# Kernel tuning notes

Measured on AMD Instinct MI355X. Metric: run time of the kernel, lower is better.

Reference implementation:

```python
import jax, jax.numpy as jnp
import numpy as np

D_MODEL = 512
D_ATTN = 128


def setup_inputs() -> dict:
    key = jax.random.key(0)
    k1, k2, k3, k4, k5 = jax.random.split(key, 5)
    B, N = 4, 4096
    x = jax.random.normal(k1, (B, N, D_MODEL), dtype=jnp.float32)
    key_mask = jnp.ones((B, N, 1), dtype=jnp.float32)
    # nn.Linear params (stored as [in, out] for x @ W)
    W_qkv = jax.random.normal(k2, (D_MODEL, 3 * D_ATTN), dtype=jnp.float32) / np.sqrt(D_MODEL)
    b_qkv = jax.random.normal(k3, (3 * D_ATTN,), dtype=jnp.float32) * 0.01
    W_out = jax.random.normal(k4, (D_ATTN, D_MODEL), dtype=jnp.float32) / np.sqrt(D_ATTN)
    b_out = jax.random.normal(k5, (D_MODEL,), dtype=jnp.float32) * 0.01
    return {"x": x, "key_mask": key_mask, "W_qkv": W_qkv, "b_qkv": b_qkv,
            "W_out": W_out, "b_out": b_out}


def reference(x, key_mask, W_qkv, b_qkv, W_out, b_out):
    # Fused QKV projection: [B, N, 3*d_attn]
    qkv = jnp.einsum('bnd,de->bne', x, W_qkv) + b_qkv
    q, k, v = jnp.split(qkv, 3, axis=-1)  # each [B, N, d_attn]
    d_attn = q.shape[-1]
    scale = 1.0 / np.sqrt(d_attn)
    # Full [B, N, N] score matrix (faithful to original einsum)
    scores = jnp.einsum('bnd,bmd->bnm', q, k)
    # Causal mask applied BEFORE scaling (as in original: mask, then *scale)
    N = x.shape[1]
    causal = jnp.tril(jnp.ones((N, N), dtype=bool))  # True = keep
    scores = jnp.where(causal[None, :, :], scores, -jnp.inf)
    scores = scores * scale
    attn = jax.nn.softmax(scores, axis=-1)  # dropout is identity in eval
    out = jnp.einsum('bnm,bmd->bnd', attn, v)
    out = out * key_mask  # broadcast [B, N, 1]
    out = jnp.einsum('bnd,de->bne', out, W_out) + b_out
    return out
```

## Files before the change

kernel.cpp:

```cpp
#include <hip/hip_runtime.h>
#include <hip/hip_bf16.h>
#include <math.h>

typedef __attribute__((ext_vector_type(4))) float f32x4;
typedef __attribute__((ext_vector_type(4))) float fvec4;
typedef __attribute__((ext_vector_type(8))) short bf16x8_t;
typedef __attribute__((ext_vector_type(4))) short bf16x4_t;

static constexpr int BATCH = 4;
static constexpr int SEQ = 4096;
static constexpr int DM = 512;
static constexpr int DA = 128;
static constexpr int BN = BATCH * SEQ;
static constexpr int IPB = 187;
static constexpr int N_ITEMS = BATCH * IPB;

static constexpr float MASKV = -3.0e38f;
static constexpr float MINIT = -1.0e30f;

static __device__ __forceinline__ unsigned short f2bf(float f) {
  unsigned u = __builtin_bit_cast(unsigned, f);
  u += 0x7fffu + ((u >> 16) & 1u);
  return (unsigned short)(u >> 16);
}
static __device__ __forceinline__ float bf2f(unsigned short u) {
  return __builtin_bit_cast(float, ((unsigned)u) << 16);
}
static __device__ __forceinline__ float fexp2(float x) {
#if __has_builtin(__builtin_amdgcn_exp2f)
  return __builtin_amdgcn_exp2f(x);
#else
  return exp2f(x);
#endif
}
static __device__ __forceinline__ unsigned pkbf(float lo, float hi) {
  unsigned r;
  asm("v_cvt_pk_bf16_f32 %0, %1, %2" : "=v"(r) : "v"(lo), "v"(hi));
  return r;
}

#define GLDS16(gsrc, ldst)                                                        \
  __builtin_amdgcn_global_load_lds(                                               \
      (const __attribute__((address_space(1))) void*)(gsrc),                      \
      (__attribute__((address_space(3))) void*)(ldst), 16, 0, 0)

static constexpr float QSC = 0.08838834764831845f * 1.4426950408889634f;

__global__ __launch_bounds__(256) void prep_kernel(
    const float* __restrict__ x, const float* __restrict__ Wqkv,
    const float* __restrict__ Wout, unsigned short* __restrict__ xbf,
    unsigned short* __restrict__ WqT, unsigned short* __restrict__ WoT) {
  long long i = ((long long)blockIdx.x * 256 + threadIdx.x) * 8;
  if (i < (long long)BN * DM) {
    fvec4 a = *(const fvec4*)&x[i];
    fvec4 b = *(const fvec4*)&x[i + 4];
    union { bf16x8_t v; unsigned short u[8]; } pk;
    pk.u[0] = f2bf(a[0]); pk.u[1] = f2bf(a[1]); pk.u[2] = f2bf(a[2]); pk.u[3] = f2bf(a[3]);
    pk.u[4] = f2bf(b[0]); pk.u[5] = f2bf(b[1]); pk.u[6] = f2bf(b[2]); pk.u[7] = f2bf(b[3]);
    *(bf16x8_t*)&xbf[i] = pk.v;
  }
  int t = blockIdx.x * 256 + threadIdx.x;
  if (t < 512 * 384) {
    int k = t / 384, n = t - k * 384;
    WqT[n * 512 + k] = f2bf(Wqkv[t]);
  }
  if (t < 128 * 512) {
    int k = t >> 9, n = t & 511;
    WoT[n * 128 + k] = f2bf(Wout[t]);
  }
}

__global__ __launch_bounds__(512, 4) void qkv_kernel(
    const unsigned short* __restrict__ xbf, const unsigned short* __restrict__ WqT,
    const float* __restrict__ bias, unsigned short* __restrict__ qbf,
    unsigned short* __restrict__ kpk, unsigned short* __restrict__ vpk) {
  __shared__ unsigned short Alds[128 * 64];
  __shared__ unsigned short Blds[128 * 64];

  const int m0 = blockIdx.x * 128;
  const int n0 = blockIdx.y * 128;
  const int tid = threadIdx.x;
  const int wave = tid >> 6, lane = tid & 63;
  const int g = lane >> 4, lr = lane & 15;
  const int wm = wave >> 2, wn = wave & 3;

  const int srow = lane >> 3;
  const int sslot = lane & 7;
  const int sksw = ((sslot ^ srow) * 8);

  f32x4 acc[4][2] = {};

  for (int kb = 0; kb < DM; kb += 64) {
    __syncthreads();
#pragma unroll
    for (int i = 0; i < 2; ++i) {
      int ch = wave * 2 + i;
      GLDS16(&xbf[(size_t)(m0 + ch * 8 + srow) * DM + kb + sksw],
             (char*)Alds + ch * 1024);
      GLDS16(&WqT[(size_t)(n0 + ch * 8 + srow) * DM + kb + sksw],
             (char*)Blds + ch * 1024);
    }
    asm volatile("s_waitcnt vmcnt(0)" ::: "memory");
    __syncthreads();

#pragma unroll
    for (int c2 = 0; c2 < 2; ++c2) {
      bf16x8_t ar[4], br[2];
#pragma unroll
      for (int mi = 0; mi < 4; ++mi) {
        int row = wm * 64 + mi * 16 + lr;
        ar[mi] = *(const bf16x8_t*)&Alds[row * 64 + (((c2 * 4 + g) ^ (row & 7)) * 8)];
      }
#pragma unroll
      for (int ni = 0; ni < 2; ++ni) {
        int row = wn * 32 + ni * 16 + lr;
        br[ni] = *(const bf16x8_t*)&Blds[row * 64 + (((c2 * 4 + g) ^ (row & 7)) * 8)];
      }
#pragma unroll
      for (int mi = 0; mi < 4; ++mi)
#pragma unroll
        for (int ni = 0; ni < 2; ++ni)
          acc[mi][ni] = __builtin_amdgcn_mfma_f32_16x16x32_bf16(ar[mi], br[ni],
                                                                acc[mi][ni], 0, 0, 0);
    }
  }

  if (n0 == 0) {
#pragma unroll
    for (int ni = 0; ni < 2; ++ni) {
      int col = wn * 32 + ni * 16 + lr;
      float bv = bias[col];
#pragma unroll
      for (int mi = 0; mi < 4; ++mi) {
        int tokb = m0 + wm * 64 + mi * 16 + 4 * g;
#pragma unroll
        for (int r = 0; r < 4; ++r)
          qbf[(size_t)(tokb + r) * DA + col] = f2bf((acc[mi][ni][r] + bv) * QSC);
      }
    }
  } else if (n0 == 128) {
#pragma unroll
    for (int ni = 0; ni < 2; ++ni) {
      int kd = wn * 32 + ni * 16 + lr;
      float bv = bias[128 + kd];
      int unit = (kd >> 5) * 4 + ((kd >> 3) & 3);
      int elem = kd & 7;
#pragma unroll
      for (int mi = 0; mi < 4; ++mi) {
        int tokb = m0 + wm * 64 + mi * 16 + 4 * g;
#pragma unroll
        for (int r = 0; r < 4; ++r) {
          int token = tokb + r;
          int tile32 = token >> 5;
          int u = (((token >> 4) & 1) * 16) + unit;
          kpk[(size_t)tile32 * 4096 + u * 128 + (token & 15) * 8 + elem] =
              f2bf(acc[mi][ni][r] + bv);
        }
      }
    }
  } else {
#pragma unroll
    for (int mi = 0; mi < 4; ++mi) {
      int keyb = m0 + wm * 64 + mi * 16 + 4 * g;
      int tile32 = keyb >> 5;
      int kl0 = keyb & 31;
      int gp = (kl0 >> 2) & 3;
      int jhi = kl0 >> 4;
#pragma unroll
      for (int ni = 0; ni < 2; ++ni) {
        int d = wn * 32 + ni * 16 + lr;
        float bv = bias[256 + d];
        union { bf16x4_t v; unsigned short u[4]; } pk;
#pragma unroll
        for (int r = 0; r < 4; ++r) pk.u[r] = f2bf(acc[mi][ni][r] + bv);
        int unit = (d >> 4) * 4 + gp;
        *(bf16x4_t*)&vpk[(size_t)tile32 * 4096 + unit * 128 + (d & 15) * 8 + jhi * 4] =
            pk.v;
      }
    }
  }
}

static __device__ __forceinline__ void softmax64(
    f32x4 s[4], float& m_r, float& l_r, f32x4* oacc, bf16x8_t pb[2]) {
  float tmax = MASKV;
#pragma unroll
  for (int ct = 0; ct < 4; ++ct)
#pragma unroll
    for (int r = 0; r < 4; ++r) tmax = fmaxf(tmax, s[ct][r]);
  tmax = fmaxf(tmax, __shfl_xor(tmax, 16, 64));
  tmax = fmaxf(tmax, __shfl_xor(tmax, 32, 64));
  if (!__all(tmax <= m_r + 10.0f)) {
    float mn = fmaxf(m_r, tmax);
    float al = fexp2(m_r - mn);
    m_r = mn;
    l_r *= al;
#pragma unroll
    for (int t = 0; t < 8; ++t)
#pragma unroll
      for (int r = 0; r < 4; ++r) oacc[t][r] *= al;
  }
  float rs = 0.f;
#pragma unroll
  for (int ct = 0; ct < 4; ++ct)
#pragma unroll
    for (int r = 0; r < 4; ++r) {
      float p = fexp2(s[ct][r] - m_r);
      s[ct][r] = p;
      rs += p;
    }
  rs += __shfl_xor(rs, 16, 64);
  rs += __shfl_xor(rs, 32, 64);
  l_r += rs;
#pragma unroll
  for (int h = 0; h < 2; ++h) {
    union { unsigned u[4]; bf16x8_t v; } pk;
    pk.u[0] = pkbf(s[2 * h][0], s[2 * h][1]);
    pk.u[1] = pkbf(s[2 * h][2], s[2 * h][3]);
    pk.u[2] = pkbf(s[2 * h + 1][0], s[2 * h + 1][1]);
    pk.u[3] = pkbf(s[2 * h + 1][2], s[2 * h + 1][3]);
    pb[h] = pk.v;
  }
}

__global__ __launch_bounds__(256, 3) void attn_kernel(
    const unsigned short* __restrict__ qbf, const unsigned short* __restrict__ kpk,
    const unsigned short* __restrict__ vpk, const float* __restrict__ key_mask,
    unsigned short* __restrict__ part_o, float* __restrict__ part_ml,
    unsigned short* __restrict__ ctx) {
  __shared__ unsigned short Klds[2][8192];
  __shared__ unsigned short Vlds[8192];

  const int flat = blockIdx.x;
  const int b = flat & 3;
  const int idxr = flat >> 2;
  int rem = idxr;
  int qb = 31;
  for (;;) {
    int nc = (qb + 3) / 3;
    if (rem < nc) break;
    rem -= nc;
    --qb;
  }
  const int ci = rem;
  const bool direct = (qb < 3);
  const int key0 = ci * 384;
  const int nkeys = min(384, (qb + 1) * 128 - key0);
  const int nt = nkeys >> 6;

  const int tid = threadIdx.x;
  const int wave = tid >> 6, lane = tid & 63;
  const int g = lane >> 4, lr = lane & 15;
  const int q0 = wave * 16 + lr;
  const int q1 = q0 + 64;

  bf16x8_t qf0[4], qf1[4];
  {
    const unsigned short* qbase = qbf + ((size_t)(b * SEQ + qb * 128)) * DA + g * 8;
#pragma unroll
    for (int c = 0; c < 4; ++c) {
      qf0[c] = *(const bf16x8_t*)(qbase + (size_t)q0 * DA + c * 32);
      qf1[c] = *(const bf16x8_t*)(qbase + (size_t)q1 * DA + c * 32);
    }
  }

  f32x4 oacc0[8] = {}, oacc1[8] = {};
  float m0r = MINIT, l0 = 0.f, m1r = MINIT, l1 = 0.f;

  const int t32b = b * 128 + ci * 12;
  const unsigned short* ksrc = kpk + (size_t)t32b * 4096 + wave * 2048 + lane * 8;
  const unsigned short* vsrc = vpk + (size_t)t32b * 4096 + wave * 2048 + lane * 8;

#define STAGEK(buf, tt)                                                      \
  do {                                                                       \
    char* kd_ = (char*)Klds[buf] + wave * 4096;                              \
    _Pragma("unroll")                                                        \
    for (int i_ = 0; i_ < 4; ++i_)                                           \
      GLDS16(ksrc + (size_t)(tt) * 8192 + i_ * 512, kd_ + i_ * 1024);        \
  } while (0)
#define STAGEV(tt)                                                           \
  do {                                                                       \
    char* vd_ = (char*)Vlds + wave * 4096;                                   \
    _Pragma("unroll")                                                        \
    for (int i_ = 0; i_ < 4; ++i_)                                           \
      GLDS16(vsrc + (size_t)(tt) * 8192 + i_ * 512, vd_ + i_ * 1024);        \
  } while (0)

  STAGEK(0, 0);

  for (int tt = 0; tt < nt; ++tt) {
    const int cur = tt & 1;
    STAGEV(tt);
    if (tt + 1 < nt) {
      STAGEK(cur ^ 1, tt + 1);
      asm volatile("s_waitcnt vmcnt(8)" ::: "memory");
    } else {
      asm volatile("s_waitcnt vmcnt(4)" ::: "memory");
    }
    __builtin_amdgcn_s_barrier();
    __builtin_amdgcn_sched_barrier(0);

    f32x4 s0[4] = {}, s1[4] = {};
    __builtin_amdgcn_s_setprio(1);
#pragma unroll
    for (int ct = 0; ct < 4; ++ct)
#pragma unroll
      for (int c = 0; c < 4; ++c) {
        bf16x8_t kf = *(const bf16x8_t*)&Klds[cur][(ct >> 1) * 4096 +
                                                   (((ct & 1) * 16 + c * 4 + g) * 16 + lr) * 8];
        s0[ct] = __builtin_amdgcn_mfma_f32_16x16x32_bf16(kf, qf0[c], s0[ct], 0, 0, 0);
        s1[ct] = __builtin_amdgcn_mfma_f32_16x16x32_bf16(kf, qf1[c], s1[ct], 0, 0, 0);
      }
    __builtin_amdgcn_s_setprio(0);

    const int koff = key0 + tt * 64 - qb * 128;
    if (koff + 63 > wave * 16) {
      int thr = q0 - koff;
#pragma unroll
      for (int ct = 0; ct < 4; ++ct)
#pragma unroll
        for (int r = 0; r < 4; ++r)
          if (16 * ct + 4 * g + r > thr) s0[ct][r] = MASKV;
    }
    if (koff + 63 > 64 + wave * 16) {
      int thr = q1 - koff;
#pragma unroll
      for (int ct = 0; ct < 4; ++ct)
#pragma unroll
        for (int r = 0; r < 4; ++r)
          if (16 * ct + 4 * g + r > thr) s1[ct][r] = MASKV;
    }

    bf16x8_t pb0[2], pb1[2];
    softmax64(s0, m0r, l0, oacc0, pb0);
    softmax64(s1, m1r, l1, oacc1, pb1);

    if (tt + 1 < nt) {
      asm volatile("s_waitcnt vmcnt(4)" ::: "memory");
    } else {
      asm volatile("s_waitcnt vmcnt(0)" ::: "memory");
    }
    __builtin_amdgcn_s_barrier();
    __builtin_amdgcn_sched_barrier(0);

    __builtin_amdgcn_s_setprio(1);
#pragma unroll
    for (int t = 0; t < 8; ++t)
#pragma unroll
      for (int h = 0; h < 2; ++h) {
        bf16x8_t vf = *(const bf16x8_t*)&Vlds[h * 4096 + ((t * 4 + g) * 16 + lr) * 8];
        oacc0[t] = __builtin_amdgcn_mfma_f32_16x16x32_bf16(vf, pb0[h], oacc0[t], 0, 0, 0);
        oacc1[t] = __builtin_amdgcn_mfma_f32_16x16x32_bf16(vf, pb1[h], oacc1[t], 0, 0, 0);
      }
    __builtin_amdgcn_s_setprio(0);

    __builtin_amdgcn_s_barrier();
  }
#undef STAGEK
#undef STAGEV

  const int slot = b * IPB + idxr;
#pragma unroll
  for (int grp = 0; grp < 2; ++grp) {
    const int row = grp ? q1 : q0;
    const f32x4* oa = grp ? oacc1 : oacc0;
    const float mr = grp ? m1r : m0r;
    const float lr_ = grp ? l1 : l0;
    if (direct) {
      float km = key_mask[b * SEQ + qb * 128 + row];
      float inv = km / lr_;
      unsigned short* co = ctx + ((size_t)(b * SEQ + qb * 128 + row)) * DA;
#pragma unroll
      for (int t = 0; t < 8; ++t) {
        union { bf16x4_t v; unsigned short u[4]; } pk;
#pragma unroll
        for (int r = 0; r < 4; ++r) pk.u[r] = f2bf(oa[t][r] * inv);
        *(bf16x4_t*)&co[t * 16 + 4 * g] = pk.v;
      }
    } else {
      unsigned short* po = part_o + (size_t)slot * 16384 + (size_t)row * 128;
#pragma unroll
      for (int t = 0; t < 8; ++t) {
        union { bf16x4_t v; unsigned short u[4]; } pk;
#pragma unroll
        for (int r = 0; r < 4; ++r) pk.u[r] = f2bf(oa[t][r]);
        *(bf16x4_t*)&po[t * 16 + 4 * g] = pk.v;
      }
      if (g == 0) {
        float2 ml = make_float2(mr, lr_);
        *(float2*)&part_ml[((size_t)slot * 128 + row) * 2] = ml;
      }
    }
  }
}

__global__ __launch_bounds__(512) void combine_kernel(
    const unsigned short* __restrict__ part_o, const float* __restrict__ part_ml,
    const float* __restrict__ key_mask, unsigned short* __restrict__ ctx) {
  const int qb = 3 + blockIdx.x;
  const int b = blockIdx.y;
  const int nc = (qb + 3) / 3;
  int idx0 = 0;
  for (int q = 31; q > qb; --q) idx0 += (q + 3) / 3;
  const int row = threadIdx.x >> 2, cg = threadIdx.x & 3;

  float m = MINIT;
  for (int ci = 0; ci < nc; ++ci) {
    int slot = b * IPB + idx0 + ci;
    m = fmaxf(m, part_ml[((size_t)slot * 128 + row) * 2 + 0]);
  }
  float l = 0.f;
  float acc[32];
#pragma unroll
  for (int k = 0; k < 32; ++k) acc[k] = 0.f;
  for (int ci = 0; ci < nc; ++ci) {
    int slot = b * IPB + idx0 + ci;
    float mi = part_ml[((size_t)slot * 128 + row) * 2 + 0];
    float li = part_ml[((size_t)slot * 128 + row) * 2 + 1];
    float w = fexp2(mi - m);
    l += w * li;
    const unsigned short* po = part_o + (size_t)slot * 16384 + (size_t)row * 128 + cg * 32;
#pragma unroll
    for (int k8 = 0; k8 < 4; ++k8) {
      bf16x8_t v = *(const bf16x8_t*)(po + k8 * 8);
#pragma unroll
      for (int jj = 0; jj < 8; ++jj)
        acc[k8 * 8 + jj] += w * bf2f((unsigned short)v[jj]);
    }
  }
  int rowg = b * SEQ + qb * 128 + row;
  float sc = key_mask[rowg] / l;
  unsigned short* co = ctx + (size_t)rowg * 128 + cg * 32;
#pragma unroll
  for (int k8 = 0; k8 < 4; ++k8) {
    union { bf16x8_t v; unsigned short u[8]; } pk;
#pragma unroll
    for (int jj = 0; jj < 8; ++jj) pk.u[jj] = f2bf(acc[k8 * 8 + jj] * sc);
    *(bf16x8_t*)(co + k8 * 8) = pk.v;
  }
}

__global__ __launch_bounds__(256) void outproj_kernel(
    const unsigned short* __restrict__ ctx, const unsigned short* __restrict__ WoT,
    const float* __restrict__ bias, float* __restrict__ out) {
  __shared__ unsigned short Alds[64 * 32];
  __shared__ unsigned short Blds[64 * 32];

  const int m0 = blockIdx.x * 64;
  const int n0 = blockIdx.y * 64;
  const int tid = threadIdx.x;
  const int wave = tid >> 6, lane = tid & 63;
  const int g = lane >> 4, lr = lane & 15;
  const int sar = tid >> 2, sak = tid & 3;
  const int sbc = tid & 63, sbk = tid >> 6;

  f32x4 acc[4] = {};

  for (int kb = 0; kb < DA; kb += 32) {
    __syncthreads();
    {
      bf16x8_t v = *(const bf16x8_t*)&ctx[(size_t)(m0 + sar) * DA + kb + sak * 8];
      *(bf16x8_t*)&Alds[(((sar >> 4) * 4 + sak) * 16 + (sar & 15)) * 8] = v;
    }
    {
      bf16x8_t v = *(const bf16x8_t*)&WoT[(size_t)(n0 + sbc) * DA + kb + sbk * 8];
      *(bf16x8_t*)&Blds[(((sbc >> 4) * 4 + sbk) * 16 + (sbc & 15)) * 8] = v;
    }
    __syncthreads();
    bf16x8_t af = *(const bf16x8_t*)&Alds[((wave * 4 + g) * 16 + lr) * 8];
#pragma unroll
    for (int c = 0; c < 4; ++c) {
      bf16x8_t bfr = *(const bf16x8_t*)&Blds[((c * 4 + g) * 16 + lr) * 8];
      acc[c] = __builtin_amdgcn_mfma_f32_16x16x32_bf16(af, bfr, acc[c], 0, 0, 0);
    }
  }

  const int rowb = m0 + wave * 16 + g * 4;
#pragma unroll
  for (int c = 0; c < 4; ++c) {
    int col = n0 + c * 16 + lr;
    float bv = bias[col];
#pragma unroll
    for (int r = 0; r < 4; ++r)
      out[(size_t)(rowb + r) * DM + col] = acc[c][r] + bv;
  }
}

extern "C" void kernel_launch(void* const* d_in, const int* in_sizes, int n_in,
                              void* d_out, int out_size, void* d_ws, size_t ws_size,
                              hipStream_t stream) {
  const float* x = (const float*)d_in[0];
  const float* key_mask = (const float*)d_in[1];
  const float* W_qkv = (const float*)d_in[2];
  const float* b_qkv = (const float*)d_in[3];
  const float* W_out = (const float*)d_in[4];
  const float* b_out = (const float*)d_in[5];
  float* out = (float*)d_out;

  unsigned short* ws = (unsigned short*)d_ws;
  unsigned short* qbf = ws;
  unsigned short* kpk = qbf + (size_t)BN * DA;
  unsigned short* vpk = kpk + (size_t)BN * DA;
  unsigned short* ctx = vpk + (size_t)BN * DA;
  unsigned short* xbf = ctx + (size_t)BN * DA;
  unsigned short* WqT = xbf + (size_t)BN * DM;
  unsigned short* WoT = WqT + (size_t)384 * 512;
  unsigned short* part_o = WoT + (size_t)512 * 128;
  float* part_ml = (float*)(part_o + (size_t)N_ITEMS * 16384);

  prep_kernel<<<dim3((BN * DM / 8 + 255) / 256), 256, 0, stream>>>(
      x, W_qkv, W_out, xbf, WqT, WoT);
  qkv_kernel<<<dim3(BN / 128, 3), 512, 0, stream>>>(xbf, WqT, b_qkv, qbf, kpk, vpk);
  attn_kernel<<<dim3(N_ITEMS), 256, 0, stream>>>(qbf, kpk, vpk, key_mask,
                                                 part_o, part_ml, ctx);
  combine_kernel<<<dim3(29, 4), 512, 0, stream>>>(part_o, part_ml, key_mask, ctx);
  outproj_kernel<<<dim3(BN / 64, 8), 256, 0, stream>>>(ctx, WoT, b_out, out);
}
```

Before: 84.74 us.

## Widen combine parallelism and retile output projection to 128x128 with swizzled async LDS loads

```diff
diff --git a/kernel.cpp b/kernel.cpp
--- a/kernel.cpp
+++ b/kernel.cpp
@@ -397,12 +397,14 @@
 __global__ __launch_bounds__(512) void combine_kernel(
     const unsigned short* __restrict__ part_o, const float* __restrict__ part_ml,
     const float* __restrict__ key_mask, unsigned short* __restrict__ ctx) {
-  const int qb = 3 + blockIdx.x;
+  const int qb = 3 + (blockIdx.x >> 2);
+  const int rq = blockIdx.x & 3;
   const int b = blockIdx.y;
   const int nc = (qb + 3) / 3;
   int idx0 = 0;
   for (int q = 31; q > qb; --q) idx0 += (q + 3) / 3;
-  const int row = threadIdx.x >> 2, cg = threadIdx.x & 3;
+  const int row = rq * 32 + (threadIdx.x >> 4);
+  const int cs = threadIdx.x & 15;
 
   float m = MINIT;
   for (int ci = 0; ci < nc; ++ci) {
@@ -410,79 +412,94 @@
     m = fmaxf(m, part_ml[((size_t)slot * 128 + row) * 2 + 0]);
   }
   float l = 0.f;
-  float acc[32];
-#pragma unroll
-  for (int k = 0; k < 32; ++k) acc[k] = 0.f;
+  float acc[8];
+#pragma unroll
+  for (int k = 0; k < 8; ++k) acc[k] = 0.f;
   for (int ci = 0; ci < nc; ++ci) {
     int slot = b * IPB + idx0 + ci;
     float mi = part_ml[((size_t)slot * 128 + row) * 2 + 0];
     float li = part_ml[((size_t)slot * 128 + row) * 2 + 1];
     float w = fexp2(mi - m);
     l += w * li;
-    const unsigned short* po = part_o + (size_t)slot * 16384 + (size_t)row * 128 + cg * 32;
-#pragma unroll
-    for (int k8 = 0; k8 < 4; ++k8) {
-      bf16x8_t v = *(const bf16x8_t*)(po + k8 * 8);
-#pragma unroll
-      for (int jj = 0; jj < 8; ++jj)
-        acc[k8 * 8 + jj] += w * bf2f((unsigned short)v[jj]);
-    }
+    const unsigned short* po =
+        part_o + (size_t)slot * 16384 + (size_t)row * 128 + cs * 8;
+    bf16x8_t v = *(const bf16x8_t*)po;
+#pragma unroll
+    for (int jj = 0; jj < 8; ++jj) acc[jj] += w * bf2f((unsigned short)v[jj]);
   }
   int rowg = b * SEQ + qb * 128 + row;
   float sc = key_mask[rowg] / l;
-  unsigned short* co = ctx + (size_t)rowg * 128 + cg * 32;
-#pragma unroll
-  for (int k8 = 0; k8 < 4; ++k8) {
-    union { bf16x8_t v; unsigned short u[8]; } pk;
-#pragma unroll
-    for (int jj = 0; jj < 8; ++jj) pk.u[jj] = f2bf(acc[k8 * 8 + jj] * sc);
-    *(bf16x8_t*)(co + k8 * 8) = pk.v;
-  }
-}
-
-__global__ __launch_bounds__(256) void outproj_kernel(
+  union { bf16x8_t v; unsigned short u[8]; } pk;
+#pragma unroll
+  for (int jj = 0; jj < 8; ++jj) pk.u[jj] = f2bf(acc[jj] * sc);
+  *(bf16x8_t*)&ctx[(size_t)rowg * 128 + cs * 8] = pk.v;
+}
+
+__global__ __launch_bounds__(512, 4) void outproj_kernel(
     const unsigned short* __restrict__ ctx, const unsigned short* __restrict__ WoT,
     const float* __restrict__ bias, float* __restrict__ out) {
-  __shared__ unsigned short Alds[64 * 32];
-  __shared__ unsigned short Blds[64 * 32];
-
-  const int m0 = blockIdx.x * 64;
-  const int n0 = blockIdx.y * 64;
+  __shared__ unsigned short Alds[128 * 64];
+  __shared__ unsigned short Blds[128 * 64];
+
+  const int m0 = blockIdx.x * 128;
+  const int n0 = blockIdx.y * 128;
   const int tid = threadIdx.x;
   const int wave = tid >> 6, lane = tid & 63;
   const int g = lane >> 4, lr = lane & 15;
-  const int sar = tid >> 2, sak = tid & 3;
-  const int sbc = tid & 63, sbk = tid >> 6;
-
-  f32x4 acc[4] = {};
-
-  for (int kb = 0; kb < DA; kb += 32) {
+  const int wm = wave >> 2, wn = wave & 3;
+
+  const int srow = lane >> 3;
+  const int sslot = lane & 7;
+  const int sksw = ((sslot ^ srow) * 8);
+
+  f32x4 acc[4][2] = {};
+
+  for (int kb = 0; kb < DA; kb += 64) {
     __syncthreads();
-    {
-      bf16x8_t v = *(const bf16x8_t*)&ctx[(size_t)(m0 + sar) * DA + kb + sak * 8];
-      *(bf16x8_t*)&Alds[(((sar >> 4) * 4 + sak) * 16 + (sar & 15)) * 8] = v;
-    }
-    {
-      bf16x8_t v = *(const bf16x8_t*)&WoT[(size_t)(n0 + sbc) * DA + kb + sbk * 8];
-      *(bf16x8_t*)&Blds[(((sbc >> 4) * 4 + sbk) * 16 + (sbc & 15)) * 8] = v;
-    }
+#pragma unroll
+    for (int i = 0; i < 2; ++i) {
+      int ch = wave * 2 + i;
+      GLDS16(&ctx[(size_t)(m0 + ch * 8 + srow) * DA + kb + sksw],
+             (char*)Alds + ch * 1024);
+      GLDS16(&WoT[(size_t)(n0 + ch * 8 + srow) * DA + kb + sksw],
+             (char*)Blds + ch * 1024);
+    }
+    asm volatile("s_waitcnt vmcnt(0)" ::: "memory");
     __syncthreads();
-    bf16x8_t af = *(const bf16x8_t*)&Alds[((wave * 4 + g) * 16 + lr) * 8];
-#pragma unroll
-    for (int c = 0; c < 4; ++c) {
-      bf16x8_t bfr = *(const bf16x8_t*)&Blds[((c * 4 + g) * 16 + lr) * 8];
-      acc[c] = __builtin_amdgcn_mfma_f32_16x16x32_bf16(af, bfr, acc[c], 0, 0, 0);
-    }
-  }
-
-  const int rowb = m0 + wave * 16 + g * 4;
-#pragma unroll
-  for (int c = 0; c < 4; ++c) {
-    int col = n0 + c * 16 + lr;
+
+#pragma unroll
+    for (int c2 = 0; c2 < 2; ++c2) {
+      bf16x8_t ar[4], br[2];
+#pragma unroll
+      for (int mi = 0; mi < 4; ++mi) {
+        int row = wm * 64 + mi * 16 + lr;
+        ar[mi] = *(const bf16x8_t*)&Alds[row * 64 + (((c2 * 4 + g) ^ (row & 7)) * 8)];
+      }
+#pragma unroll
+      for (int ni = 0; ni < 2; ++ni) {
+        int row = wn * 32 + ni * 16 + lr;
+        br[ni] = *(const bf16x8_t*)&Blds[row * 64 + (((c2 * 4 + g) ^ (row & 7)) * 8)];
+      }
+#pragma unroll
+      for (int mi = 0; mi < 4; ++mi)
+#pragma unroll
+        for (int ni = 0; ni < 2; ++ni)
+          acc[mi][ni] = __builtin_amdgcn_mfma_f32_16x16x32_bf16(ar[mi], br[ni],
+                                                                acc[mi][ni], 0, 0, 0);
+    }
+  }
+
+#pragma unroll
+  for (int ni = 0; ni < 2; ++ni) {
+    int col = n0 + wn * 32 + ni * 16 + lr;
     float bv = bias[col];
 #pragma unroll
-    for (int r = 0; r < 4; ++r)
-      out[(size_t)(rowb + r) * DM + col] = acc[c][r] + bv;
+    for (int mi = 0; mi < 4; ++mi) {
+      int tokb = m0 + wm * 64 + mi * 16 + 4 * g;
+#pragma unroll
+      for (int r = 0; r < 4; ++r)
+        out[(size_t)(tokb + r) * DM + col] = acc[mi][ni][r] + bv;
+    }
   }
 }
 
@@ -513,6 +530,6 @@
   qkv_kernel<<<dim3(BN / 128, 3), 512, 0, stream>>>(xbf, WqT, b_qkv, qbf, kpk, vpk);
   attn_kernel<<<dim3(N_ITEMS), 256, 0, stream>>>(qbf, kpk, vpk, key_mask,
                                                  part_o, part_ml, ctx);
-  combine_kernel<<<dim3(29, 4), 512, 0, stream>>>(part_o, part_ml, key_mask, ctx);
-  outproj_kernel<<<dim3(BN / 64, 8), 256, 0, stream>>>(ctx, WoT, b_out, out);
-}
+  combine_kernel<<<dim3(29 * 4, 4), 512, 0, stream>>>(part_o, part_ml, key_mask, ctx);
+  outproj_kernel<<<dim3(BN / 128, 4), 512, 0, stream>>>(ctx, WoT, b_out, out);
+}
```

Result: faster. 75.54 us (median of 3 runs) (-10.9%).
